# Kernel tuning notes

Hardware: AMD Instinct MI355X
Metric: run time of the kernel (lower is better)

## Reference

```python
import jax, jax.numpy as jnp
import numpy as np

N_NODES = 50000
N_EDGES = 800000
IN_CH = 128
HID = 64
NUM_HEADS = 8
NUM_CLASSES = 2
NEG_SLOPE = 0.2   # PyG GATConv default LeakyReLU slope
BN_EPS = 1e-5
SOFTMAX_EPS = 1e-16  # PyG softmax denominator epsilon


def setup_inputs() -> dict:
    key = jax.random.key(0)
    ks = jax.random.split(key, 20)
    s = 0.1
    inp = {
        "x": jax.random.normal(ks[0], (N_NODES, IN_CH), dtype=jnp.float32),
        "edge_index": jax.random.randint(ks[1], (2, N_EDGES), 0, N_NODES, dtype=jnp.int64),
        # layer 0 params, stacked over the 8 independent heads
        "W0": jax.random.normal(ks[2], (NUM_HEADS, IN_CH, HID), dtype=jnp.float32) * s,
        "a_src0": jax.random.normal(ks[3], (NUM_HEADS, HID), dtype=jnp.float32) * s,
        "a_dst0": jax.random.normal(ks[4], (NUM_HEADS, HID), dtype=jnp.float32) * s,
        "b0": jnp.zeros((NUM_HEADS, HID), dtype=jnp.float32),
        "gamma0": jnp.ones((NUM_HEADS, HID), dtype=jnp.float32),
        "beta0": jnp.zeros((NUM_HEADS, HID), dtype=jnp.float32),
        # layer 1 params
        "W1": jax.random.normal(ks[5], (NUM_HEADS, HID, HID), dtype=jnp.float32) * s,
        "a_src1": jax.random.normal(ks[6], (NUM_HEADS, HID), dtype=jnp.float32) * s,
        "a_dst1": jax.random.normal(ks[7], (NUM_HEADS, HID), dtype=jnp.float32) * s,
        "b1": jnp.zeros((NUM_HEADS, HID), dtype=jnp.float32),
        "gamma1": jnp.ones((NUM_HEADS, HID), dtype=jnp.float32),
        "beta1": jnp.zeros((NUM_HEADS, HID), dtype=jnp.float32),
        # ensemble classifier
        "Wc": jax.random.normal(ks[8], (NUM_HEADS * HID, NUM_CLASSES), dtype=jnp.float32) * s,
        "bc": jnp.zeros((NUM_CLASSES,), dtype=jnp.float32),
    }
    return inp


def _gat_layer(x, src, dst, n, W, a_s, a_d, b):
    """Single-head GATConv (PyG semantics, self-loops already in src/dst)."""
    h = x @ W                                           # [N, C]
    logits = (h @ a_s)[src] + (h @ a_d)[dst]            # [E]
    logits = jax.nn.leaky_relu(logits, NEG_SLOPE)
    m = jax.ops.segment_max(logits, dst, num_segments=n)
    ex = jnp.exp(logits - m[dst])
    denom = jax.ops.segment_sum(ex, dst, num_segments=n)
    alpha = ex / (denom[dst] + SOFTMAX_EPS)             # segment softmax over dst
    out = jax.ops.segment_sum(h[src] * alpha[:, None], dst, num_segments=n)
    return out + b


def _bn(h, gamma, beta):
    # BatchNorm1d training-mode math (batch statistics over nodes)
    mu = jnp.mean(h, axis=0)
    var = jnp.var(h, axis=0)
    return (h - mu) * jax.lax.rsqrt(var + BN_EPS) * gamma + beta


def reference(x, edge_index, W0, a_src0, a_dst0, b0, gamma0, beta0,
              W1, a_src1, a_dst1, b1, gamma1, beta1, Wc, bc):
    n = x.shape[0]
    loops = jnp.arange(n, dtype=edge_index.dtype)
    src = jnp.concatenate([edge_index[0], loops])  # PyG add_self_loops=True
    dst = jnp.concatenate([edge_index[1], loops])

    def branch(Wh0, as0, ad0, bh0, g0, be0, Wh1, as1, ad1, bh1, g1, be1):
        h = _gat_layer(x, src, dst, n, Wh0, as0, ad0, bh0)
        h = jax.nn.elu(_bn(h, g0, be0))                  # dropout off (eval)
        h = _gat_layer(h, src, dst, n, Wh1, as1, ad1, bh1)
        h = jax.nn.elu(_bn(h, g1, be1))
        return h                                          # [N, HID]

    hs = jax.vmap(branch)(W0, a_src0, a_dst0, b0, gamma0, beta0,
                          W1, a_src1, a_dst1, b1, gamma1, beta1)  # [H, N, HID]
    feat = jnp.transpose(hs, (1, 0, 2)).reshape(n, -1)            # [N, H*HID]
    return feat @ Wc + bc
```

## Files before the change

kernel.cpp:

```cpp
#include <hip/hip_runtime.h>
#include <hip/hip_bf16.h>
#include <math.h>
#include <stdint.h>

#define N_NODES 50000
#define N_EDGES 800000
#define E_TOT   (N_EDGES + N_NODES)
#define IN_CH   128
#define HID     64
#define NHEAD   8
#define C       512
#define NEG_SLOPE 0.2f
#define BN_EPS    1e-5f
#define SM_EPS    1e-16f
#define SCAN_B    196
#define STAT_B    256

typedef __attribute__((ext_vector_type(8))) short bf16x8;
typedef __attribute__((ext_vector_type(4))) float f32x4;

__device__ __forceinline__ float lrelu(float x){ return x > 0.f ? x : NEG_SLOPE * x; }
__device__ __forceinline__ float elu(float x){ return x > 0.f ? x : __expf(x) - 1.f; }
__device__ __forceinline__ float bflo(unsigned u){ return __uint_as_float(u << 16); }
__device__ __forceinline__ float bfhi(unsigned u){ return __uint_as_float(u & 0xffff0000u); }
__device__ __forceinline__ float bfu(unsigned short u){ return __uint_as_float(((unsigned)u) << 16); }
__device__ __forceinline__ unsigned short f2bf(float f){
  unsigned u = __float_as_uint(f);
  unsigned r = u + 0x7fffu + ((u >> 16) & 1u);
  return (unsigned short)(r >> 16);
}

__global__ void k_detect(const int* __restrict__ ei, int* flag){
  if (threadIdx.x == 0 && blockIdx.x == 0) {
    int f = 1;
    for (int i = 0; i < 32; i++) if (ei[2*i + 1] != 0) f = 0;
    *flag = f;
  }
}
__global__ void k_init_counts(int* counts){
  int i = blockIdx.x * 256 + threadIdx.x;
  if (i < N_NODES) counts[i] = 1;
}
__global__ void k_extract_count(const int* __restrict__ ei, const int* __restrict__ flag,
                                int* __restrict__ src32, int* __restrict__ dst32,
                                int* counts){
  int e = blockIdx.x * 256 + threadIdx.x;
  if (e >= N_EDGES) return;
  int s, d;
  if (*flag) {
    const long long* e64 = (const long long*)ei;
    s = (int)e64[e];
    d = (int)e64[(size_t)N_EDGES + e];
  } else {
    s = ei[e];
    d = ei[N_EDGES + e];
  }
  src32[e] = s; dst32[e] = d;
  atomicAdd(&counts[d], 1);
}

__global__ void k_scan1(const int* __restrict__ counts, int* __restrict__ excl, int* __restrict__ bsum){
  __shared__ int s[256];
  int tid = threadIdx.x;
  int i = blockIdx.x * 256 + tid;
  int v = (i < N_NODES) ? counts[i] : 0;
  s[tid] = v; __syncthreads();
#pragma unroll
  for (int d = 1; d < 256; d <<= 1) {
    int t = (tid >= d) ? s[tid - d] : 0;
    __syncthreads(); s[tid] += t; __syncthreads();
  }
  if (i < N_NODES) excl[i] = s[tid] - v;
  if (tid == 255) bsum[blockIdx.x] = s[255];
}
__global__ void k_scan2(int* bsum){
  __shared__ int s[256];
  int tid = threadIdx.x;
  int v = (tid < SCAN_B) ? bsum[tid] : 0;
  s[tid] = v; __syncthreads();
#pragma unroll
  for (int d = 1; d < 256; d <<= 1) {
    int t = (tid >= d) ? s[tid - d] : 0;
    __syncthreads(); s[tid] += t; __syncthreads();
  }
  if (tid < SCAN_B) bsum[tid] = s[tid] - v;
}
__global__ void k_scan3(const int* __restrict__ excl, const int* __restrict__ bsum,
                        int* __restrict__ off, int* __restrict__ cursor, int* __restrict__ csr){
  int i = blockIdx.x * 256 + threadIdx.x;
  if (i < N_NODES) {
    int o = excl[i] + bsum[blockIdx.x];
    off[i] = o; cursor[i] = o + 1; csr[o] = i;
  }
  if (i == 0) off[N_NODES] = E_TOT;
}
__global__ void k_scatter_edges(const int* __restrict__ src, const int* __restrict__ dst,
                                int* cursor, int* __restrict__ csr_src){
  int e = blockIdx.x * 256 + threadIdx.x;
  if (e < N_EDGES) { int d = dst[e]; int p = atomicAdd(&cursor[d], 1); csr_src[p] = src[e]; }
}

template<int K>
__global__ void k_transpose_w(const float* __restrict__ W, unsigned short* __restrict__ Bt){
  int i = blockIdx.x * 256 + threadIdx.x;
  int k = i % K; int rem = i / K; int c = rem & 63; int h = rem >> 6;
  Bt[i] = f2bf(W[((size_t)h * K + k) * 64 + c]);
}

__global__ __launch_bounds__(256) void k_gemm0(const float* __restrict__ X,
                                               const unsigned short* __restrict__ Bt,
                                               const float* __restrict__ a_src,
                                               const float* __restrict__ a_dst,
                                               unsigned short* __restrict__ H16,
                                               float* __restrict__ s_src,
                                               float* __restrict__ s_dst){
  __shared__ unsigned short LA[64 * 136];
  __shared__ unsigned short LB[64 * 136];
  int r0 = blockIdx.x * 64;
  int tid = threadIdx.x;
#pragma unroll
  for (int i = 0; i < 4; i++) {
    int idx = tid + i * 256;
    int r = idx >> 4, l16 = idx & 15;
    float4 u0 = make_float4(0.f,0.f,0.f,0.f), u1 = u0;
    if (r0 + r < N_NODES) {
      const float* xp = &X[(size_t)(r0 + r) * IN_CH + l16 * 8];
      u0 = *reinterpret_cast<const float4*>(xp);
      u1 = *reinterpret_cast<const float4*>(xp + 4);
    }
    ushort4 p0, p1;
    p0.x = f2bf(u0.x); p0.y = f2bf(u0.y); p0.z = f2bf(u0.z); p0.w = f2bf(u0.w);
    p1.x = f2bf(u1.x); p1.y = f2bf(u1.y); p1.z = f2bf(u1.z); p1.w = f2bf(u1.w);
    *reinterpret_cast<ushort4*>(&LA[r * 136 + l16 * 8]) = p0;
    *reinterpret_cast<ushort4*>(&LA[r * 136 + l16 * 8 + 4]) = p1;
  }
  int w = tid >> 6, l = tid & 63;
  int lr = l & 15, lg = l >> 4;
  for (int h = 0; h < NHEAD; h++) {
    __syncthreads();
#pragma unroll
    for (int i = 0; i < 4; i++) {
      int idx = tid + i * 256;
      int c = idx >> 4, l16 = idx & 15;
      uint4 v = *reinterpret_cast<const uint4*>(&Bt[(size_t)h * 8192 + c * 128 + l16 * 8]);
      *reinterpret_cast<uint4*>(&LB[c * 136 + l16 * 8]) = v;
    }
    __syncthreads();
    f32x4 acc[4] = {};
#pragma unroll
    for (int kf = 0; kf < 4; kf++) {
      bf16x8 af = *reinterpret_cast<const bf16x8*>(&LA[(w * 16 + lr) * 136 + kf * 32 + lg * 8]);
#pragma unroll
      for (int cf = 0; cf < 4; cf++) {
        bf16x8 bfr = *reinterpret_cast<const bf16x8*>(&LB[(cf * 16 + lr) * 136 + kf * 32 + lg * 8]);
        acc[cf] = __builtin_amdgcn_mfma_f32_16x16x32_bf16(af, bfr, acc[cf], 0, 0, 0);
      }
    }
#pragma unroll
    for (int cf = 0; cf < 4; cf++)
#pragma unroll
      for (int rr = 0; rr < 4; rr++) {
        int gr = r0 + w * 16 + lg * 4 + rr;
        if (gr < N_NODES)
          H16[(size_t)gr * C + h * HID + cf * 16 + lr] = f2bf(acc[cf][rr]);
      }
    float ps[4] = {}, pd[4] = {};
#pragma unroll
    for (int cf = 0; cf < 4; cf++) {
      float as_ = a_src[h * HID + cf * 16 + lr];
      float ad_ = a_dst[h * HID + cf * 16 + lr];
#pragma unroll
      for (int rr = 0; rr < 4; rr++) { ps[rr] += acc[cf][rr] * as_; pd[rr] += acc[cf][rr] * ad_; }
    }
#pragma unroll
    for (int rr = 0; rr < 4; rr++)
#pragma unroll
      for (int o = 1; o < 16; o <<= 1) { ps[rr] += __shfl_xor(ps[rr], o, 64); pd[rr] += __shfl_xor(pd[rr], o, 64); }
    if (lr == 0) {
#pragma unroll
      for (int rr = 0; rr < 4; rr++) {
        int gr = r0 + w * 16 + lg * 4 + rr;
        if (gr < N_NODES) { s_src[gr * NHEAD + h] = ps[rr]; s_dst[gr * NHEAD + h] = pd[rr]; }
      }
    }
  }
}

__global__ __launch_bounds__(256) void k_gemm1(const unsigned short* __restrict__ Hb,
                                               const unsigned short* __restrict__ Bt,
                                               const float* __restrict__ scale,
                                               const float* __restrict__ shift,
                                               const float* __restrict__ a_src,
                                               const float* __restrict__ a_dst,
                                               unsigned short* __restrict__ H16,
                                               float* __restrict__ s_src,
                                               float* __restrict__ s_dst){
  __shared__ unsigned short LA[64 * 72];
  __shared__ unsigned short LB[64 * 72];
  int r0 = blockIdx.x * 64, h = blockIdx.y;
  int tid = threadIdx.x;
#pragma unroll
  for (int i = 0; i < 4; i++) {
    int idx = tid + i * 256;
    int r = idx >> 4, l16 = idx & 15;
    ushort4 hv = make_ushort4(0, 0, 0, 0);
    if (r0 + r < N_NODES)
      hv = *reinterpret_cast<const ushort4*>(&Hb[(size_t)(r0 + r) * C + h * HID + l16 * 4]);
    float4 sc = *reinterpret_cast<const float4*>(&scale[h * HID + l16 * 4]);
    float4 sh = *reinterpret_cast<const float4*>(&shift[h * HID + l16 * 4]);
    ushort4 p;
    p.x = f2bf(elu(sc.x * bfu(hv.x) + sh.x));
    p.y = f2bf(elu(sc.y * bfu(hv.y) + sh.y));
    p.z = f2bf(elu(sc.z * bfu(hv.z) + sh.z));
    p.w = f2bf(elu(sc.w * bfu(hv.w) + sh.w));
    *reinterpret_cast<ushort4*>(&LA[r * 72 + l16 * 4]) = p;
  }
#pragma unroll
  for (int i = 0; i < 2; i++) {
    int idx = tid + i * 256;
    int c = idx >> 3, l8 = idx & 7;
    uint4 v = *reinterpret_cast<const uint4*>(&Bt[(size_t)h * 4096 + c * 64 + l8 * 8]);
    *reinterpret_cast<uint4*>(&LB[c * 72 + l8 * 8]) = v;
  }
  __syncthreads();
  int w = tid >> 6, l = tid & 63;
  int lr = l & 15, lg = l >> 4;
  f32x4 acc[4] = {};
#pragma unroll
  for (int kf = 0; kf < 2; kf++) {
    bf16x8 af = *reinterpret_cast<const bf16x8*>(&LA[(w * 16 + lr) * 72 + kf * 32 + lg * 8]);
#pragma unroll
    for (int cf = 0; cf < 4; cf++) {
      bf16x8 bfr = *reinterpret_cast<const bf16x8*>(&LB[(cf * 16 + lr) * 72 + kf * 32 + lg * 8]);
      acc[cf] = __builtin_amdgcn_mfma_f32_16x16x32_bf16(af, bfr, acc[cf], 0, 0, 0);
    }
  }
#pragma unroll
  for (int cf = 0; cf < 4; cf++)
#pragma unroll
    for (int rr = 0; rr < 4; rr++) {
      int gr = r0 + w * 16 + lg * 4 + rr;
      if (gr < N_NODES)
        H16[(size_t)gr * C + h * HID + cf * 16 + lr] = f2bf(acc[cf][rr]);
    }
  float ps[4] = {}, pd[4] = {};
#pragma unroll
  for (int cf = 0; cf < 4; cf++) {
    float as_ = a_src[h * HID + cf * 16 + lr];
    float ad_ = a_dst[h * HID + cf * 16 + lr];
#pragma unroll
    for (int rr = 0; rr < 4; rr++) { ps[rr] += acc[cf][rr] * as_; pd[rr] += acc[cf][rr] * ad_; }
  }
#pragma unroll
  for (int rr = 0; rr < 4; rr++)
#pragma unroll
    for (int o = 1; o < 16; o <<= 1) { ps[rr] += __shfl_xor(ps[rr], o, 64); pd[rr] += __shfl_xor(pd[rr], o, 64); }
  if (lr == 0) {
#pragma unroll
    for (int rr = 0; rr < 4; rr++) {
      int gr = r0 + w * 16 + lg * 4 + rr;
      if (gr < N_NODES) { s_src[gr * NHEAD + h] = ps[rr]; s_dst[gr * NHEAD + h] = pd[rr]; }
    }
  }
}

__global__ __launch_bounds__(256) void k_aggregate(const unsigned short* __restrict__ H16,
                                                   const float* __restrict__ s_src,
                                                   const float* __restrict__ s_dst,
                                                   const int* __restrict__ off,
                                                   const int* __restrict__ csr,
                                                   const float* __restrict__ bias,
                                                   unsigned short* __restrict__ HoutB){
  __shared__ float aexp[4][64][8];
  __shared__ int   sidx[4][64];
  int wv = threadIdx.x >> 6, lane = threadIdx.x & 63;
  int n = blockIdx.x * 4 + wv;
  if (n >= N_NODES) return;
  int e0 = off[n], deg = off[n + 1] - e0;
  int hsel = lane >> 3;

  float sd[NHEAD];
#pragma unroll
  for (int h = 0; h < NHEAD; h++) sd[h] = s_dst[n * NHEAD + h];

  float acc[8] = {};
  float dnl[NHEAD] = {};

  for (int base = 0; base < deg; base += 64) {
    int e = base + lane;
    int cnt = min(64, deg - base);
    if (e < deg) {
      int s = csr[e0 + e];
      sidx[wv][lane] = s;
      const float4* sp = reinterpret_cast<const float4*>(&s_src[s * NHEAD]);
      float4 s01 = sp[0], s23 = sp[1];
      float sv[8] = { s01.x, s01.y, s01.z, s01.w, s23.x, s23.y, s23.z, s23.w };
#pragma unroll
      for (int h = 0; h < NHEAD; h++) {
        float ex = __expf(lrelu(sv[h] + sd[h]));
        dnl[h] += ex;
        aexp[wv][lane][h] = ex;
      }
    }
    int j = 0;
    for (; j + 4 <= cnt; j += 4) {
      int s0 = sidx[wv][j+0], s1 = sidx[wv][j+1], s2 = sidx[wv][j+2], s3 = sidx[wv][j+3];
      float a0 = aexp[wv][j+0][hsel], a1 = aexp[wv][j+1][hsel];
      float a2 = aexp[wv][j+2][hsel], a3 = aexp[wv][j+3][hsel];
      uint4 v0 = reinterpret_cast<const uint4*>(H16 + (size_t)s0 * C)[lane];
      uint4 v1 = reinterpret_cast<const uint4*>(H16 + (size_t)s1 * C)[lane];
      uint4 v2 = reinterpret_cast<const uint4*>(H16 + (size_t)s2 * C)[lane];
      uint4 v3 = reinterpret_cast<const uint4*>(H16 + (size_t)s3 * C)[lane];
      acc[0] += a0 * bflo(v0.x); acc[1] += a0 * bfhi(v0.x);
      acc[2] += a0 * bflo(v0.y); acc[3] += a0 * bfhi(v0.y);
      acc[4] += a0 * bflo(v0.z); acc[5] += a0 * bfhi(v0.z);
      acc[6] += a0 * bflo(v0.w); acc[7] += a0 * bfhi(v0.w);
      acc[0] += a1 * bflo(v1.x); acc[1] += a1 * bfhi(v1.x);
      acc[2] += a1 * bflo(v1.y); acc[3] += a1 * bfhi(v1.y);
      acc[4] += a1 * bflo(v1.z); acc[5] += a1 * bfhi(v1.z);
      acc[6] += a1 * bflo(v1.w); acc[7] += a1 * bfhi(v1.w);
      acc[0] += a2 * bflo(v2.x); acc[1] += a2 * bfhi(v2.x);
      acc[2] += a2 * bflo(v2.y); acc[3] += a2 * bfhi(v2.y);
      acc[4] += a2 * bflo(v2.z); acc[5] += a2 * bfhi(v2.z);
      acc[6] += a2 * bflo(v2.w); acc[7] += a2 * bfhi(v2.w);
      acc[0] += a3 * bflo(v3.x); acc[1] += a3 * bfhi(v3.x);
      acc[2] += a3 * bflo(v3.y); acc[3] += a3 * bfhi(v3.y);
      acc[4] += a3 * bflo(v3.z); acc[5] += a3 * bfhi(v3.z);
      acc[6] += a3 * bflo(v3.w); acc[7] += a3 * bfhi(v3.w);
    }
    for (; j < cnt; j++) {
      int s = sidx[wv][j];
      float a = aexp[wv][j][hsel];
      uint4 v = reinterpret_cast<const uint4*>(H16 + (size_t)s * C)[lane];
      acc[0] += a * bflo(v.x); acc[1] += a * bfhi(v.x);
      acc[2] += a * bflo(v.y); acc[3] += a * bfhi(v.y);
      acc[4] += a * bflo(v.z); acc[5] += a * bfhi(v.z);
      acc[6] += a * bflo(v.w); acc[7] += a * bfhi(v.w);
    }
  }

  float mydn = 0.f;
#pragma unroll
  for (int h = 0; h < NHEAD; h++) {
    float d = dnl[h];
#pragma unroll
    for (int o = 32; o; o >>= 1) d += __shfl_xor(d, o, 64);
    if (hsel == h) mydn = d;
  }
  float inv = 1.f / (mydn + SM_EPS);

  const float* bp = bias + lane * 8;
  ushort4 p0, p1;
  p0.x = f2bf(acc[0]*inv + bp[0]); p0.y = f2bf(acc[1]*inv + bp[1]);
  p0.z = f2bf(acc[2]*inv + bp[2]); p0.w = f2bf(acc[3]*inv + bp[3]);
  p1.x = f2bf(acc[4]*inv + bp[4]); p1.y = f2bf(acc[5]*inv + bp[5]);
  p1.z = f2bf(acc[6]*inv + bp[6]); p1.w = f2bf(acc[7]*inv + bp[7]);
  unsigned short* op = HoutB + (size_t)n * C + lane * 8;
  *reinterpret_cast<ushort4*>(op) = p0;
  *reinterpret_cast<ushort4*>(op + 4) = p1;
}

__global__ __launch_bounds__(256) void k_bn_stats(const unsigned short* __restrict__ Hb,
                                                  float* __restrict__ partial){
  __shared__ float red[4][64][16];
  int tid = threadIdx.x, w = tid >> 6, c64 = tid & 63;
  float s[8] = {}, q[8] = {};
  for (int r = blockIdx.x * 4 + w; r < N_NODES; r += gridDim.x * 4) {
    uint4 v = *reinterpret_cast<const uint4*>(&Hb[(size_t)r * C + c64 * 8]);
    float f[8] = { bflo(v.x), bfhi(v.x), bflo(v.y), bfhi(v.y),
                   bflo(v.z), bfhi(v.z), bflo(v.w), bfhi(v.w) };
#pragma unroll
    for (int k = 0; k < 8; k++) { s[k] += f[k]; q[k] += f[k] * f[k]; }
  }
#pragma unroll
  for (int k = 0; k < 8; k++) { red[w][c64][k] = s[k]; red[w][c64][k + 8] = q[k]; }
  __syncthreads();
  if (w == 0) {
#pragma unroll
    for (int k = 0; k < 8; k++) {
      float ss = red[0][c64][k] + red[1][c64][k] + red[2][c64][k] + red[3][c64][k];
      float qq = red[0][c64][k+8] + red[1][c64][k+8] + red[2][c64][k+8] + red[3][c64][k+8];
      partial[(size_t)blockIdx.x * 1024 + c64 * 8 + k] = ss;
      partial[(size_t)blockIdx.x * 1024 + 512 + c64 * 8 + k] = qq;
    }
  }
}
__global__ void k_bn_finalize(const float* __restrict__ partial, const float* __restrict__ gamma,
                              const float* __restrict__ beta, float* __restrict__ scale,
                              float* __restrict__ shift){
  int c = threadIdx.x;
  float s = 0.f, q = 0.f;
  for (int b = 0; b < STAT_B; b++) {
    s += partial[(size_t)b * 1024 + c];
    q += partial[(size_t)b * 1024 + 512 + c];
  }
  float mean = s * (1.f / N_NODES);
  float var  = q * (1.f / N_NODES) - mean * mean;
  float sc = gamma[c] * rsqrtf(var + BN_EPS);
  scale[c] = sc;
  shift[c] = beta[c] - mean * sc;
}

__global__ __launch_bounds__(256) void k_final(const unsigned short* __restrict__ Hb,
                                               const float* __restrict__ scale,
                                               const float* __restrict__ shift,
                                               const float* __restrict__ Wc,
                                               const float* __restrict__ bc,
                                               float* __restrict__ out){
  int wave = threadIdx.x >> 6, lane = threadIdx.x & 63;
  int n = blockIdx.x * 4 + wave;
  if (n >= N_NODES) return;
  uint4 v = *reinterpret_cast<const uint4*>(&Hb[(size_t)n * C + lane * 8]);
  float f[8] = { bflo(v.x), bfhi(v.x), bflo(v.y), bfhi(v.y),
                 bflo(v.z), bfhi(v.z), bflo(v.w), bfhi(v.w) };
  float4 sc0 = *reinterpret_cast<const float4*>(&scale[lane * 8]);
  float4 sc1 = *reinterpret_cast<const float4*>(&scale[lane * 8 + 4]);
  float4 sh0 = *reinterpret_cast<const float4*>(&shift[lane * 8]);
  float4 sh1 = *reinterpret_cast<const float4*>(&shift[lane * 8 + 4]);
  float scv[8] = { sc0.x, sc0.y, sc0.z, sc0.w, sc1.x, sc1.y, sc1.z, sc1.w };
  float shv[8] = { sh0.x, sh0.y, sh0.z, sh0.w, sh1.x, sh1.y, sh1.z, sh1.w };
  float a0 = 0.f, a1 = 0.f;
#pragma unroll
  for (int k = 0; k < 8; k++) {
    float t = elu(scv[k] * f[k] + shv[k]);
    int ch = lane * 8 + k;
    a0 += t * Wc[ch * 2 + 0];
    a1 += t * Wc[ch * 2 + 1];
  }
#pragma unroll
  for (int o = 32; o; o >>= 1) { a0 += __shfl_xor(a0, o, 64); a1 += __shfl_xor(a1, o, 64); }
  if (lane == 0) { out[n * 2 + 0] = a0 + bc[0]; out[n * 2 + 1] = a1 + bc[1]; }
}

extern "C" void kernel_launch(void* const* d_in, const int* in_sizes, int n_in,
                              void* d_out, int out_size, void* d_ws, size_t ws_size,
                              hipStream_t stream) {
  const float* x      = (const float*)d_in[0];
  const int*   ei     = (const int*)d_in[1];
  const float* W0     = (const float*)d_in[2];
  const float* a_src0 = (const float*)d_in[3];
  const float* a_dst0 = (const float*)d_in[4];
  const float* b0     = (const float*)d_in[5];
  const float* gamma0 = (const float*)d_in[6];
  const float* beta0  = (const float*)d_in[7];
  const float* W1     = (const float*)d_in[8];
  const float* a_src1 = (const float*)d_in[9];
  const float* a_dst1 = (const float*)d_in[10];
  const float* b1     = (const float*)d_in[11];
  const float* gamma1 = (const float*)d_in[12];
  const float* beta1  = (const float*)d_in[13];
  const float* Wc     = (const float*)d_in[14];
  const float* bc     = (const float*)d_in[15];
  float* out = (float*)d_out;

  char* ws = (char*)d_ws;
  size_t o = 0;
  auto alloc = [&](size_t bytes) { char* p = ws + o; o = (o + bytes + 255) & ~(size_t)255; return p; };
  int*   flag    = (int*)  alloc(4);
  int*   src32   = (int*)  alloc((size_t)N_EDGES * 4);
  int*   dst32   = (int*)  alloc((size_t)N_EDGES * 4);
  int*   counts  = (int*)  alloc((size_t)N_NODES * 4);
  int*   excl    = (int*)  alloc((size_t)N_NODES * 4);
  int*   bsum    = (int*)  alloc(256 * 4);
  int*   off     = (int*)  alloc((size_t)(N_NODES + 1) * 4);
  int*   cursor  = (int*)  alloc((size_t)N_NODES * 4);
  int*   csr     = (int*)  alloc((size_t)E_TOT * 4);
  float* s_src   = (float*)alloc((size_t)N_NODES * NHEAD * 4);
  float* s_dst   = (float*)alloc((size_t)N_NODES * NHEAD * 4);
  float* partial = (float*)alloc((size_t)STAT_B * 1024 * 4);
  float* scale   = (float*)alloc(C * 4);
  float* shift   = (float*)alloc(C * 4);
  unsigned short* bt0  = (unsigned short*)alloc((size_t)NHEAD * HID * IN_CH * 2);
  unsigned short* bt1  = (unsigned short*)alloc((size_t)NHEAD * HID * HID * 2);
  unsigned short* h16a = (unsigned short*)alloc((size_t)N_NODES * C * 2);
  unsigned short* h16b = (unsigned short*)alloc((size_t)N_NODES * C * 2);

  const int GE = (N_EDGES + 255) / 256;
  const int GN = (N_NODES + 255) / 256;
  const int GW = (N_NODES + 3) / 4;
  const int GR = (N_NODES + 63) / 64;

  k_detect<<<1, 64, 0, stream>>>(ei, flag);
  k_init_counts<<<GN, 256, 0, stream>>>(counts);
  k_extract_count<<<GE, 256, 0, stream>>>(ei, flag, src32, dst32, counts);

  k_transpose_w<IN_CH><<<(NHEAD * HID * IN_CH + 255) / 256, 256, 0, stream>>>(W0, bt0);
  k_transpose_w<HID><<<(NHEAD * HID * HID + 255) / 256, 256, 0, stream>>>(W1, bt1);

  k_scan1<<<GN, 256, 0, stream>>>(counts, excl, bsum);
  k_scan2<<<1, 256, 0, stream>>>(bsum);
  k_scan3<<<GN, 256, 0, stream>>>(excl, bsum, off, cursor, csr);
  k_scatter_edges<<<GE, 256, 0, stream>>>(src32, dst32, cursor, csr);

  k_gemm0<<<GR, 256, 0, stream>>>(x, bt0, a_src0, a_dst0, h16a, s_src, s_dst);
  k_aggregate<<<GW, 256, 0, stream>>>(h16a, s_src, s_dst, off, csr, b0, h16b);
  k_bn_stats<<<STAT_B, 256, 0, stream>>>(h16b, partial);
  k_bn_finalize<<<1, 512, 0, stream>>>(partial, gamma0, beta0, scale, shift);

  k_gemm1<<<dim3(GR, NHEAD), 256, 0, stream>>>(h16b, bt1, scale, shift, a_src1, a_dst1, h16a, s_src, s_dst);
  k_aggregate<<<GW, 256, 0, stream>>>(h16a, s_src, s_dst, off, csr, b1, h16b);
  k_bn_stats<<<STAT_B, 256, 0, stream>>>(h16b, partial);
  k_bn_finalize<<<1, 512, 0, stream>>>(partial, gamma1, beta1, scale, shift);

  k_final<<<GW, 256, 0, stream>>>(h16b, scale, shift, Wc, bc, out);
}
```

Baseline: 506.1 us.

## Pack source scores into feature rows, aggregate two nodes per wave, fuse launches

Stores each node's per-head source attention scores in a 32-byte header placed before its bf16 feature row (row length 544). The aggregation gather then reads scores and features from one row instead of a separate s_src array. The aggregation kernel now handles two destination nodes per wave with interleaved loads to raise memory-level parallelism, and takes source indices through shuffles instead of shared memory. Several small setup kernels are merged: detect and init, the two weight transposes, and scan1 with scan2 via a last-block atomic. The padded rows add memory traffic to the BN and final passes, and pairing nodes may diverge when their degrees differ.

```diff
diff --git a/kernel.cpp b/kernel.cpp
--- a/kernel.cpp
+++ b/kernel.cpp
@@ -10,6 +10,8 @@
 #define HID     64
 #define NHEAD   8
 #define C       512
+#define ROWLEN  544
+#define HDR     16
 #define NEG_SLOPE 0.2f
 #define BN_EPS    1e-5f
 #define SM_EPS    1e-16f
@@ -29,17 +31,22 @@
   unsigned r = u + 0x7fffu + ((u >> 16) & 1u);
   return (unsigned short)(r >> 16);
 }
-
-__global__ void k_detect(const int* __restrict__ ei, int* flag){
-  if (threadIdx.x == 0 && blockIdx.x == 0) {
-    int f = 1;
-    for (int i = 0; i < 32; i++) if (ei[2*i + 1] != 0) f = 0;
-    *flag = f;
-  }
-}
-__global__ void k_init_counts(int* counts){
+__device__ __forceinline__ void fma8(float* acc, float a, uint4 v){
+  acc[0] += a * bflo(v.x); acc[1] += a * bfhi(v.x);
+  acc[2] += a * bflo(v.y); acc[3] += a * bfhi(v.y);
+  acc[4] += a * bflo(v.z); acc[5] += a * bfhi(v.z);
+  acc[6] += a * bflo(v.w); acc[7] += a * bfhi(v.w);
+}
+
+__global__ void k_init(const int* __restrict__ ei, int* counts, int* flag, int* done){
   int i = blockIdx.x * 256 + threadIdx.x;
   if (i < N_NODES) counts[i] = 1;
+  if (blockIdx.x == 0 && threadIdx.x == 0) {
+    int f = 1;
+    for (int k = 0; k < 32; k++) if (ei[2*k + 1] != 0) f = 0;
+    *flag = f;
+    *done = 0;
+  }
 }
 __global__ void k_extract_count(const int* __restrict__ ei, const int* __restrict__ flag,
                                 int* __restrict__ src32, int* __restrict__ dst32,
@@ -59,8 +66,10 @@
   atomicAdd(&counts[d], 1);
 }
 
-__global__ void k_scan1(const int* __restrict__ counts, int* __restrict__ excl, int* __restrict__ bsum){
+__global__ void k_scan12(const int* __restrict__ counts, int* __restrict__ excl,
+                         int* __restrict__ bsum, int* done, int* __restrict__ bsum_s){
   __shared__ int s[256];
+  __shared__ int isLast;
   int tid = threadIdx.x;
   int i = blockIdx.x * 256 + tid;
   int v = (i < N_NODES) ? counts[i] : 0;
@@ -72,24 +81,26 @@
   }
   if (i < N_NODES) excl[i] = s[tid] - v;
   if (tid == 255) bsum[blockIdx.x] = s[255];
-}
-__global__ void k_scan2(int* bsum){
-  __shared__ int s[256];
-  int tid = threadIdx.x;
-  int v = (tid < SCAN_B) ? bsum[tid] : 0;
-  s[tid] = v; __syncthreads();
-#pragma unroll
-  for (int d = 1; d < 256; d <<= 1) {
-    int t = (tid >= d) ? s[tid - d] : 0;
-    __syncthreads(); s[tid] += t; __syncthreads();
-  }
-  if (tid < SCAN_B) bsum[tid] = s[tid] - v;
-}
-__global__ void k_scan3(const int* __restrict__ excl, const int* __restrict__ bsum,
+  __threadfence();
+  if (tid == 0) isLast = (atomicAdd(done, 1) == gridDim.x - 1);
+  __syncthreads();
+  if (isLast) {
+    __threadfence();
+    int bv = (tid < SCAN_B) ? bsum[tid] : 0;
+    s[tid] = bv; __syncthreads();
+#pragma unroll
+    for (int d = 1; d < 256; d <<= 1) {
+      int t = (tid >= d) ? s[tid - d] : 0;
+      __syncthreads(); s[tid] += t; __syncthreads();
+    }
+    if (tid < SCAN_B) bsum_s[tid] = s[tid] - bv;
+  }
+}
+__global__ void k_scan3(const int* __restrict__ excl, const int* __restrict__ bsum_s,
                         int* __restrict__ off, int* __restrict__ cursor, int* __restrict__ csr){
   int i = blockIdx.x * 256 + threadIdx.x;
   if (i < N_NODES) {
-    int o = excl[i] + bsum[blockIdx.x];
+    int o = excl[i] + bsum_s[blockIdx.x];
     off[i] = o; cursor[i] = o + 1; csr[o] = i;
   }
   if (i == 0) off[N_NODES] = E_TOT;
@@ -100,19 +111,24 @@
   if (e < N_EDGES) { int d = dst[e]; int p = atomicAdd(&cursor[d], 1); csr_src[p] = src[e]; }
 }
 
-template<int K>
-__global__ void k_transpose_w(const float* __restrict__ W, unsigned short* __restrict__ Bt){
+__global__ void k_transpose_both(const float* __restrict__ W0, const float* __restrict__ W1,
+                                 unsigned short* __restrict__ bt0, unsigned short* __restrict__ bt1){
   int i = blockIdx.x * 256 + threadIdx.x;
-  int k = i % K; int rem = i / K; int c = rem & 63; int h = rem >> 6;
-  Bt[i] = f2bf(W[((size_t)h * K + k) * 64 + c]);
+  if (i < 65536) {
+    int k = i & 127; int rem = i >> 7; int c = rem & 63; int h = rem >> 6;
+    bt0[i] = f2bf(W0[((size_t)h * IN_CH + k) * 64 + c]);
+  } else {
+    int j = i - 65536;
+    int k = j & 63; int rem = j >> 6; int c = rem & 63; int h = rem >> 6;
+    bt1[j] = f2bf(W1[((size_t)h * HID + k) * 64 + c]);
+  }
 }
 
 __global__ __launch_bounds__(256) void k_gemm0(const float* __restrict__ X,
                                                const unsigned short* __restrict__ Bt,
                                                const float* __restrict__ a_src,
                                                const float* __restrict__ a_dst,
-                                               unsigned short* __restrict__ H16,
-                                               float* __restrict__ s_src,
+                                               unsigned short* __restrict__ Hrow,
                                                float* __restrict__ s_dst){
   __shared__ unsigned short LA[64 * 136];
   __shared__ unsigned short LB[64 * 136];
@@ -162,7 +178,7 @@
       for (int rr = 0; rr < 4; rr++) {
         int gr = r0 + w * 16 + lg * 4 + rr;
         if (gr < N_NODES)
-          H16[(size_t)gr * C + h * HID + cf * 16 + lr] = f2bf(acc[cf][rr]);
+          Hrow[(size_t)gr * ROWLEN + HDR + h * HID + cf * 16 + lr] = f2bf(acc[cf][rr]);
       }
     float ps[4] = {}, pd[4] = {};
 #pragma unroll
@@ -180,7 +196,10 @@
 #pragma unroll
       for (int rr = 0; rr < 4; rr++) {
         int gr = r0 + w * 16 + lg * 4 + rr;
-        if (gr < N_NODES) { s_src[gr * NHEAD + h] = ps[rr]; s_dst[gr * NHEAD + h] = pd[rr]; }
+        if (gr < N_NODES) {
+          reinterpret_cast<float*>(&Hrow[(size_t)gr * ROWLEN])[h] = ps[rr];
+          s_dst[gr * NHEAD + h] = pd[rr];
+        }
       }
     }
   }
@@ -192,8 +211,7 @@
                                                const float* __restrict__ shift,
                                                const float* __restrict__ a_src,
                                                const float* __restrict__ a_dst,
-                                               unsigned short* __restrict__ H16,
-                                               float* __restrict__ s_src,
+                                               unsigned short* __restrict__ Hrow,
                                                float* __restrict__ s_dst){
   __shared__ unsigned short LA[64 * 72];
   __shared__ unsigned short LB[64 * 72];
@@ -205,7 +223,7 @@
     int r = idx >> 4, l16 = idx & 15;
     ushort4 hv = make_ushort4(0, 0, 0, 0);
     if (r0 + r < N_NODES)
-      hv = *reinterpret_cast<const ushort4*>(&Hb[(size_t)(r0 + r) * C + h * HID + l16 * 4]);
+      hv = *reinterpret_cast<const ushort4*>(&Hb[(size_t)(r0 + r) * ROWLEN + HDR + h * HID + l16 * 4]);
     float4 sc = *reinterpret_cast<const float4*>(&scale[h * HID + l16 * 4]);
     float4 sh = *reinterpret_cast<const float4*>(&shift[h * HID + l16 * 4]);
     ushort4 p;
@@ -241,7 +259,7 @@
     for (int rr = 0; rr < 4; rr++) {
       int gr = r0 + w * 16 + lg * 4 + rr;
       if (gr < N_NODES)
-        H16[(size_t)gr * C + h * HID + cf * 16 + lr] = f2bf(acc[cf][rr]);
+        Hrow[(size_t)gr * ROWLEN + HDR + h * HID + cf * 16 + lr] = f2bf(acc[cf][rr]);
     }
   float ps[4] = {}, pd[4] = {};
 #pragma unroll
@@ -259,105 +277,133 @@
 #pragma unroll
     for (int rr = 0; rr < 4; rr++) {
       int gr = r0 + w * 16 + lg * 4 + rr;
-      if (gr < N_NODES) { s_src[gr * NHEAD + h] = ps[rr]; s_dst[gr * NHEAD + h] = pd[rr]; }
-    }
-  }
-}
-
-__global__ __launch_bounds__(256) void k_aggregate(const unsigned short* __restrict__ H16,
-                                                   const float* __restrict__ s_src,
+      if (gr < N_NODES) {
+        reinterpret_cast<float*>(&Hrow[(size_t)gr * ROWLEN])[h] = ps[rr];
+        s_dst[gr * NHEAD + h] = pd[rr];
+      }
+    }
+  }
+}
+
+__global__ __launch_bounds__(256) void k_aggregate(const unsigned short* __restrict__ Hin,
                                                    const float* __restrict__ s_dst,
                                                    const int* __restrict__ off,
                                                    const int* __restrict__ csr,
                                                    const float* __restrict__ bias,
-                                                   unsigned short* __restrict__ HoutB){
-  __shared__ float aexp[4][64][8];
-  __shared__ int   sidx[4][64];
+                                                   unsigned short* __restrict__ Hout){
+  __shared__ float aexp[4][2][64][8];
   int wv = threadIdx.x >> 6, lane = threadIdx.x & 63;
-  int n = blockIdx.x * 4 + wv;
-  if (n >= N_NODES) return;
-  int e0 = off[n], deg = off[n + 1] - e0;
+  int nA = blockIdx.x * 8 + wv * 2;
+  if (nA >= N_NODES) return;
+  int nB = nA + 1;
+  int e0A = off[nA], degA = off[nA + 1] - e0A;
+  int e0B = off[nB], degB = off[nB + 1] - e0B;
   int hsel = lane >> 3;
 
-  float sd[NHEAD];
-#pragma unroll
-  for (int h = 0; h < NHEAD; h++) sd[h] = s_dst[n * NHEAD + h];
-
-  float acc[8] = {};
-  float dnl[NHEAD] = {};
-
-  for (int base = 0; base < deg; base += 64) {
-    int e = base + lane;
-    int cnt = min(64, deg - base);
-    if (e < deg) {
-      int s = csr[e0 + e];
-      sidx[wv][lane] = s;
-      const float4* sp = reinterpret_cast<const float4*>(&s_src[s * NHEAD]);
-      float4 s01 = sp[0], s23 = sp[1];
+  float sdA[NHEAD], sdB[NHEAD];
+  {
+    const float4* pa = reinterpret_cast<const float4*>(&s_dst[nA * NHEAD]);
+    const float4* pb = reinterpret_cast<const float4*>(&s_dst[nB * NHEAD]);
+    float4 a0 = pa[0], a1 = pa[1], b0 = pb[0], b1 = pb[1];
+    sdA[0]=a0.x; sdA[1]=a0.y; sdA[2]=a0.z; sdA[3]=a0.w; sdA[4]=a1.x; sdA[5]=a1.y; sdA[6]=a1.z; sdA[7]=a1.w;
+    sdB[0]=b0.x; sdB[1]=b0.y; sdB[2]=b0.z; sdB[3]=b0.w; sdB[4]=b1.x; sdB[5]=b1.y; sdB[6]=b1.z; sdB[7]=b1.w;
+  }
+
+  float accA[8] = {}, accB[8] = {};
+  float dnlA[NHEAD] = {}, dnlB[NHEAD] = {};
+  int maxdeg = max(degA, degB);
+
+  for (int base = 0; base < maxdeg; base += 64) {
+    int cntA = min(64, max(0, degA - base));
+    int cntB = min(64, max(0, degB - base));
+    int sregA = 0, sregB = 0;
+    if (lane < cntA) {
+      sregA = csr[e0A + base + lane];
+      const float* hp = reinterpret_cast<const float*>(Hin + (size_t)sregA * ROWLEN);
+      float4 s01 = reinterpret_cast<const float4*>(hp)[0];
+      float4 s23 = reinterpret_cast<const float4*>(hp)[1];
       float sv[8] = { s01.x, s01.y, s01.z, s01.w, s23.x, s23.y, s23.z, s23.w };
 #pragma unroll
       for (int h = 0; h < NHEAD; h++) {
-        float ex = __expf(lrelu(sv[h] + sd[h]));
-        dnl[h] += ex;
-        aexp[wv][lane][h] = ex;
+        float ex = __expf(lrelu(sv[h] + sdA[h]));
+        dnlA[h] += ex;
+        aexp[wv][0][lane][h] = ex;
       }
     }
+    if (lane < cntB) {
+      sregB = csr[e0B + base + lane];
+      const float* hp = reinterpret_cast<const float*>(Hin + (size_t)sregB * ROWLEN);
+      float4 s01 = reinterpret_cast<const float4*>(hp)[0];
+      float4 s23 = reinterpret_cast<const float4*>(hp)[1];
+      float sv[8] = { s01.x, s01.y, s01.z, s01.w, s23.x, s23.y, s23.z, s23.w };
+#pragma unroll
+      for (int h = 0; h < NHEAD; h++) {
+        float ex = __expf(lrelu(sv[h] + sdB[h]));
+        dnlB[h] += ex;
+        aexp[wv][1][lane][h] = ex;
+      }
+    }
+    int cm = max(cntA, cntB);
     int j = 0;
-    for (; j + 4 <= cnt; j += 4) {
-      int s0 = sidx[wv][j+0], s1 = sidx[wv][j+1], s2 = sidx[wv][j+2], s3 = sidx[wv][j+3];
-      float a0 = aexp[wv][j+0][hsel], a1 = aexp[wv][j+1][hsel];
-      float a2 = aexp[wv][j+2][hsel], a3 = aexp[wv][j+3][hsel];
-      uint4 v0 = reinterpret_cast<const uint4*>(H16 + (size_t)s0 * C)[lane];
-      uint4 v1 = reinterpret_cast<const uint4*>(H16 + (size_t)s1 * C)[lane];
-      uint4 v2 = reinterpret_cast<const uint4*>(H16 + (size_t)s2 * C)[lane];
-      uint4 v3 = reinterpret_cast<const uint4*>(H16 + (size_t)s3 * C)[lane];
-      acc[0] += a0 * bflo(v0.x); acc[1] += a0 * bfhi(v0.x);
-      acc[2] += a0 * bflo(v0.y); acc[3] += a0 * bfhi(v0.y);
-      acc[4] += a0 * bflo(v0.z); acc[5] += a0 * bfhi(v0.z);
-      acc[6] += a0 * bflo(v0.w); acc[7] += a0 * bfhi(v0.w);
-      acc[0] += a1 * bflo(v1.x); acc[1] += a1 * bfhi(v1.x);
-      acc[2] += a1 * bflo(v1.y); acc[3] += a1 * bfhi(v1.y);
-      acc[4] += a1 * bflo(v1.z); acc[5] += a1 * bfhi(v1.z);
-      acc[6] += a1 * bflo(v1.w); acc[7] += a1 * bfhi(v1.w);
-      acc[0] += a2 * bflo(v2.x); acc[1] += a2 * bfhi(v2.x);
-      acc[2] += a2 * bflo(v2.y); acc[3] += a2 * bfhi(v2.y);
-      acc[4] += a2 * bflo(v2.z); acc[5] += a2 * bfhi(v2.z);
-      acc[6] += a2 * bflo(v2.w); acc[7] += a2 * bfhi(v2.w);
-      acc[0] += a3 * bflo(v3.x); acc[1] += a3 * bfhi(v3.x);
-      acc[2] += a3 * bflo(v3.y); acc[3] += a3 * bfhi(v3.y);
-      acc[4] += a3 * bflo(v3.z); acc[5] += a3 * bfhi(v3.z);
-      acc[6] += a3 * bflo(v3.w); acc[7] += a3 * bfhi(v3.w);
-    }
-    for (; j < cnt; j++) {
-      int s = sidx[wv][j];
-      float a = aexp[wv][j][hsel];
-      uint4 v = reinterpret_cast<const uint4*>(H16 + (size_t)s * C)[lane];
-      acc[0] += a * bflo(v.x); acc[1] += a * bfhi(v.x);
-      acc[2] += a * bflo(v.y); acc[3] += a * bfhi(v.y);
-      acc[4] += a * bflo(v.z); acc[5] += a * bfhi(v.z);
-      acc[6] += a * bflo(v.w); acc[7] += a * bfhi(v.w);
-    }
-  }
-
-  float mydn = 0.f;
+    for (; j + 2 <= cm; j += 2) {
+      int iA0 = __shfl(sregA, j, 64), iA1 = __shfl(sregA, j + 1, 64);
+      int iB0 = __shfl(sregB, j, 64), iB1 = __shfl(sregB, j + 1, 64);
+      bool a0 = j < cntA, a1 = j + 1 < cntA, b0 = j < cntB, b1 = j + 1 < cntB;
+      uint4 vA0, vA1, vB0, vB1;
+      if (a0) vA0 = reinterpret_cast<const uint4*>(Hin + (size_t)iA0 * ROWLEN + HDR)[lane];
+      if (b0) vB0 = reinterpret_cast<const uint4*>(Hin + (size_t)iB0 * ROWLEN + HDR)[lane];
+      if (a1) vA1 = reinterpret_cast<const uint4*>(Hin + (size_t)iA1 * ROWLEN + HDR)[lane];
+      if (b1) vB1 = reinterpret_cast<const uint4*>(Hin + (size_t)iB1 * ROWLEN + HDR)[lane];
+      if (a0) fma8(accA, aexp[wv][0][j][hsel], vA0);
+      if (b0) fma8(accB, aexp[wv][1][j][hsel], vB0);
+      if (a1) fma8(accA, aexp[wv][0][j + 1][hsel], vA1);
+      if (b1) fma8(accB, aexp[wv][1][j + 1][hsel], vB1);
+    }
+    for (; j < cm; j++) {
+      int iA = __shfl(sregA, j, 64), iB = __shfl(sregB, j, 64);
+      bool a0 = j < cntA, b0 = j < cntB;
+      uint4 vA, vB;
+      if (a0) vA = reinterpret_cast<const uint4*>(Hin + (size_t)iA * ROWLEN + HDR)[lane];
+      if (b0) vB = reinterpret_cast<const uint4*>(Hin + (size_t)iB * ROWLEN + HDR)[lane];
+      if (a0) fma8(accA, aexp[wv][0][j][hsel], vA);
+      if (b0) fma8(accB, aexp[wv][1][j][hsel], vB);
+    }
+  }
+
+  float mydnA = 0.f, mydnB = 0.f;
 #pragma unroll
   for (int h = 0; h < NHEAD; h++) {
-    float d = dnl[h];
-#pragma unroll
-    for (int o = 32; o; o >>= 1) d += __shfl_xor(d, o, 64);
-    if (hsel == h) mydn = d;
-  }
-  float inv = 1.f / (mydn + SM_EPS);
+    float dA = dnlA[h], dB = dnlB[h];
+#pragma unroll
+    for (int o = 32; o; o >>= 1) { dA += __shfl_xor(dA, o, 64); dB += __shfl_xor(dB, o, 64); }
+    if (hsel == h) { mydnA = dA; mydnB = dB; }
+  }
+  float invA = 1.f / (mydnA + SM_EPS);
+  float invB = 1.f / (mydnB + SM_EPS);
 
   const float* bp = bias + lane * 8;
-  ushort4 p0, p1;
-  p0.x = f2bf(acc[0]*inv + bp[0]); p0.y = f2bf(acc[1]*inv + bp[1]);
-  p0.z = f2bf(acc[2]*inv + bp[2]); p0.w = f2bf(acc[3]*inv + bp[3]);
-  p1.x = f2bf(acc[4]*inv + bp[4]); p1.y = f2bf(acc[5]*inv + bp[5]);
-  p1.z = f2bf(acc[6]*inv + bp[6]); p1.w = f2bf(acc[7]*inv + bp[7]);
-  unsigned short* op = HoutB + (size_t)n * C + lane * 8;
-  *reinterpret_cast<ushort4*>(op) = p0;
-  *reinterpret_cast<ushort4*>(op + 4) = p1;
+  float b0_ = bp[0], b1_ = bp[1], b2_ = bp[2], b3_ = bp[3];
+  float b4_ = bp[4], b5_ = bp[5], b6_ = bp[6], b7_ = bp[7];
+  {
+    ushort4 p0, p1;
+    p0.x = f2bf(accA[0]*invA + b0_); p0.y = f2bf(accA[1]*invA + b1_);
+    p0.z = f2bf(accA[2]*invA + b2_); p0.w = f2bf(accA[3]*invA + b3_);
+    p1.x = f2bf(accA[4]*invA + b4_); p1.y = f2bf(accA[5]*invA + b5_);
+    p1.z = f2bf(accA[6]*invA + b6_); p1.w = f2bf(accA[7]*invA + b7_);
+    unsigned short* op = Hout + (size_t)nA * ROWLEN + HDR + lane * 8;
+    *reinterpret_cast<ushort4*>(op) = p0;
+    *reinterpret_cast<ushort4*>(op + 4) = p1;
+  }
+  {
+    ushort4 p0, p1;
+    p0.x = f2bf(accB[0]*invB + b0_); p0.y = f2bf(accB[1]*invB + b1_);
+    p0.z = f2bf(accB[2]*invB + b2_); p0.w = f2bf(accB[3]*invB + b3_);
+    p1.x = f2bf(accB[4]*invB + b4_); p1.y = f2bf(accB[5]*invB + b5_);
+    p1.z = f2bf(accB[6]*invB + b6_); p1.w = f2bf(accB[7]*invB + b7_);
+    unsigned short* op = Hout + (size_t)nB * ROWLEN + HDR + lane * 8;
+    *reinterpret_cast<ushort4*>(op) = p0;
+    *reinterpret_cast<ushort4*>(op + 4) = p1;
+  }
 }
 
 __global__ __launch_bounds__(256) void k_bn_stats(const unsigned short* __restrict__ Hb,
@@ -366,7 +412,7 @@
   int tid = threadIdx.x, w = tid >> 6, c64 = tid & 63;
   float s[8] = {}, q[8] = {};
   for (int r = blockIdx.x * 4 + w; r < N_NODES; r += gridDim.x * 4) {
-    uint4 v = *reinterpret_cast<const uint4*>(&Hb[(size_t)r * C + c64 * 8]);
+    uint4 v = *reinterpret_cast<const uint4*>(&Hb[(size_t)r * ROWLEN + HDR + c64 * 8]);
     float f[8] = { bflo(v.x), bfhi(v.x), bflo(v.y), bfhi(v.y),
                    bflo(v.z), bfhi(v.z), bflo(v.w), bfhi(v.w) };
 #pragma unroll
@@ -410,7 +456,7 @@
   int wave = threadIdx.x >> 6, lane = threadIdx.x & 63;
   int n = blockIdx.x * 4 + wave;
   if (n >= N_NODES) return;
-  uint4 v = *reinterpret_cast<const uint4*>(&Hb[(size_t)n * C + lane * 8]);
+  uint4 v = *reinterpret_cast<const uint4*>(&Hb[(size_t)n * ROWLEN + HDR + lane * 8]);
   float f[8] = { bflo(v.x), bfhi(v.x), bflo(v.y), bfhi(v.y),
                  bflo(v.z), bfhi(v.z), bflo(v.w), bfhi(v.w) };
   float4 sc0 = *reinterpret_cast<const float4*>(&scale[lane * 8]);
@@ -457,50 +503,47 @@
   size_t o = 0;
   auto alloc = [&](size_t bytes) { char* p = ws + o; o = (o + bytes + 255) & ~(size_t)255; return p; };
   int*   flag    = (int*)  alloc(4);
+  int*   done    = (int*)  alloc(4);
   int*   src32   = (int*)  alloc((size_t)N_EDGES * 4);
   int*   dst32   = (int*)  alloc((size_t)N_EDGES * 4);
   int*   counts  = (int*)  alloc((size_t)N_NODES * 4);
   int*   excl    = (int*)  alloc((size_t)N_NODES * 4);
   int*   bsum    = (int*)  alloc(256 * 4);
+  int*   bsum_s  = (int*)  alloc(256 * 4);
   int*   off     = (int*)  alloc((size_t)(N_NODES + 1) * 4);
   int*   cursor  = (int*)  alloc((size_t)N_NODES * 4);
   int*   csr     = (int*)  alloc((size_t)E_TOT * 4);
-  float* s_src   = (float*)alloc((size_t)N_NODES * NHEAD * 4);
   float* s_dst   = (float*)alloc((size_t)N_NODES * NHEAD * 4);
   float* partial = (float*)alloc((size_t)STAT_B * 1024 * 4);
   float* scale   = (float*)alloc(C * 4);
   float* shift   = (float*)alloc(C * 4);
   unsigned short* bt0  = (unsigned short*)alloc((size_t)NHEAD * HID * IN_CH * 2);
   unsigned short* bt1  = (unsigned short*)alloc((size_t)NHEAD * HID * HID * 2);
-  unsigned short* h16a = (unsigned short*)alloc((size_t)N_NODES * C * 2);
-  unsigned short* h16b = (unsigned short*)alloc((size_t)N_NODES * C * 2);
+  unsigned short* hrowA = (unsigned short*)alloc((size_t)N_NODES * ROWLEN * 2);
+  unsigned short* hrowB = (unsigned short*)alloc((size_t)N_NODES * ROWLEN * 2);
 
   const int GE = (N_EDGES + 255) / 256;
   const int GN = (N_NODES + 255) / 256;
   const int GW = (N_NODES + 3) / 4;
+  const int GA = (N_NODES + 7) / 8;
   const int GR = (N_NODES + 63) / 64;
 
-  k_detect<<<1, 64, 0, stream>>>(ei, flag);
-  k_init_counts<<<GN, 256, 0, stream>>>(counts);
+  k_init<<<GN, 256, 0, stream>>>(ei, counts, flag, done);
   k_extract_count<<<GE, 256, 0, stream>>>(ei, flag, src32, dst32, counts);
-
-  k_transpose_w<IN_CH><<<(NHEAD * HID * IN_CH + 255) / 256, 256, 0, stream>>>(W0, bt0);
-  k_transpose_w<HID><<<(NHEAD * HID * HID + 255) / 256, 256, 0, stream>>>(W1, bt1);
-
-  k_scan1<<<GN, 256, 0, stream>>>(counts, excl, bsum);
-  k_scan2<<<1, 256, 0, stream>>>(bsum);
-  k_scan3<<<GN, 256, 0, stream>>>(excl, bsum, off, cursor, csr);
+  k_transpose_both<<<384, 256, 0, stream>>>(W0, W1, bt0, bt1);
+  k_scan12<<<GN, 256, 0, stream>>>(counts, excl, bsum, done, bsum_s);
+  k_scan3<<<GN, 256, 0, stream>>>(excl, bsum_s, off, cursor, csr);
   k_scatter_edges<<<GE, 256, 0, stream>>>(src32, dst32, cursor, csr);
 
-  k_gemm0<<<GR, 256, 0, stream>>>(x, bt0, a_src0, a_dst0, h16a, s_src, s_dst);
-  k_aggregate<<<GW, 256, 0, stream>>>(h16a, s_src, s_dst, off, csr, b0, h16b);
-  k_bn_stats<<<STAT_B, 256, 0, stream>>>(h16b, partial);
+  k_gemm0<<<GR, 256, 0, stream>>>(x, bt0, a_src0, a_dst0, hrowA, s_dst);
+  k_aggregate<<<GA, 256, 0, stream>>>(hrowA, s_dst, off, csr, b0, hrowB);
+  k_bn_stats<<<STAT_B, 256, 0, stream>>>(hrowB, partial);
   k_bn_finalize<<<1, 512, 0, stream>>>(partial, gamma0, beta0, scale, shift);
 
-  k_gemm1<<<dim3(GR, NHEAD), 256, 0, stream>>>(h16b, bt1, scale, shift, a_src1, a_dst1, h16a, s_src, s_dst);
-  k_aggregate<<<GW, 256, 0, stream>>>(h16a, s_src, s_dst, off, csr, b1, h16b);
-  k_bn_stats<<<STAT_B, 256, 0, stream>>>(h16b, partial);
+  k_gemm1<<<dim3(GR, NHEAD), 256, 0, stream>>>(hrowB, bt1, scale, shift, a_src1, a_dst1, hrowA, s_dst);
+  k_aggregate<<<GA, 256, 0, stream>>>(hrowA, s_dst, off, csr, b1, hrowB);
+  k_bn_stats<<<STAT_B, 256, 0, stream>>>(hrowB, partial);
   k_bn_finalize<<<1, 512, 0, stream>>>(partial, gamma1, beta1, scale, shift);
 
-  k_final<<<GW, 256, 0, stream>>>(h16b, scale, shift, Wc, bc, out);
-}
+  k_final<<<GW, 256, 0, stream>>>(hrowB, scale, shift, Wc, bc, out);
+}
```

Result: slower. 572.9 us (+13.2%).
